# Optimization experiments

Hardware: AMD Instinct MI355X
Metric: run time of the kernel (lower is better)

## Reference

```python
import jax, jax.numpy as jnp
import numpy as np

D_MODEL = 1024
NUM_HEADS = 16
D_HEAD = D_MODEL // NUM_HEADS
MAX_SEQ_LEN = 2048
THETA = 10000.0
BATCH = 2
SEQ = 2048


def _rope_tables():
    # inv_freq over even dims; emb interleaves each freq twice: [f0,f0,f1,f1,...]
    inv_freq = 1.0 / (THETA ** (jnp.arange(0, D_HEAD, 2, dtype=jnp.float32) / D_HEAD))
    t = jnp.arange(MAX_SEQ_LEN, dtype=jnp.float32)
    freqs = jnp.einsum('i,j->ij', t, inv_freq)  # [S, d_head/2]
    emb = jnp.stack((freqs, freqs), axis=-1).reshape(MAX_SEQ_LEN, D_HEAD)
    return jnp.cos(emb), jnp.sin(emb)


def _rotate_half(x):
    # pairwise interleaved rotation: (x0,x1,x2,x3,...) -> (-x1,x0,-x3,x2,...)
    xr = x.reshape(x.shape[:-1] + (D_HEAD // 2, 2))
    x1, x2 = xr[..., 0], xr[..., 1]
    return jnp.stack((-x2, x1), axis=-1).reshape(x.shape)


def setup_inputs() -> dict:
    key = jax.random.key(0)
    ks = jax.random.split(key, 5)
    std = np.sqrt(2.0 / (D_MODEL + D_MODEL)).astype(np.float32)
    return {
        'in_features': jax.random.normal(ks[0], (BATCH, SEQ, D_MODEL), dtype=jnp.float32),
        'token_positions': jnp.arange(SEQ, dtype=jnp.int64) if jax.config.jax_enable_x64 else jnp.arange(SEQ, dtype=jnp.int32),
        'wq': jax.random.normal(ks[1], (D_MODEL, D_MODEL), dtype=jnp.float32) * std,
        'wk': jax.random.normal(ks[2], (D_MODEL, D_MODEL), dtype=jnp.float32) * std,
        'wv': jax.random.normal(ks[3], (D_MODEL, D_MODEL), dtype=jnp.float32) * std,
        'wo': jax.random.normal(ks[4], (D_MODEL, D_MODEL), dtype=jnp.float32) * std,
    }


def reference(in_features, token_positions, wq, wk, wv, wo):
    b, s, _ = in_features.shape
    cos_tab, sin_tab = _rope_tables()
    cos = cos_tab[token_positions]  # [s, d_head]
    sin = sin_tab[token_positions]

    def split_heads(t):  # [b, s, d_model] -> [b, h, s, d_head]
        return t.reshape(b, s, NUM_HEADS, D_HEAD).transpose(0, 2, 1, 3)

    q = split_heads(jnp.einsum('bsd,ed->bse', in_features, wq))
    k = split_heads(jnp.einsum('bsd,ed->bse', in_features, wk))
    v = split_heads(jnp.einsum('bsd,ed->bse', in_features, wv))

    q = q * cos + _rotate_half(q) * sin
    k = k * cos + _rotate_half(k) * sin

    scale = 1.0 / np.sqrt(D_HEAD).astype(np.float32)
    scores = jnp.einsum('bhqd,bhkd->bhqk', q, k) * scale  # [b,h,s,s]
    causal = jnp.tril(jnp.ones((s, s), dtype=bool))
    scores = jnp.where(causal, scores, -jnp.inf)
    weights = jax.nn.softmax(scores, axis=-1)
    out = jnp.einsum('bhqk,bhkd->bhqd', weights, v)
    out = out.transpose(0, 2, 1, 3).reshape(b, s, D_MODEL)
    return jnp.einsum('bsd,ed->bse', out, wo)
```

## Files before the change

### kernel.cpp

```cpp
#include <hip/hip_runtime.h>


typedef __attribute__((ext_vector_type(8))) short bf16x8;
typedef __attribute__((ext_vector_type(4))) float f32x4;

__device__ __forceinline__ short f2bf(float f) {
  unsigned u = __float_as_uint(f);
  unsigned r = (u + 0x7fffu + ((u >> 16) & 1u)) >> 16;
  return (short)(r & 0xFFFFu);
}

__device__ __forceinline__ unsigned pk2(float a, float b) {
  return __builtin_amdgcn_perm(__float_as_uint(b) + 0x8000u,
                               __float_as_uint(a) + 0x8000u, 0x07060302u);
}

__device__ __forceinline__ void async16(const void* g, void* l) {
  __builtin_amdgcn_global_load_lds(
      (const __attribute__((address_space(1))) void*)g,
      (__attribute__((address_space(3))) void*)l, 16, 0, 0);
}

__device__ __forceinline__ void cstore(short* C, size_t i, float v) { C[i] = f2bf(v); }
__device__ __forceinline__ void cstore(float* C, size_t i, float v) { C[i] = v; }

__global__ void cast_all(const float4* __restrict__ X,
                         const float4* __restrict__ w0, const float4* __restrict__ w1,
                         const float4* __restrict__ w2, const float4* __restrict__ w3,
                         short* __restrict__ Xb, short* __restrict__ Wb) {
  int t = blockIdx.x * 256 + threadIdx.x;
  const float4* s;
  short4* d;
  if (t < (1 << 20)) {
    s = X + t; d = (short4*)Xb + t;
  } else {
    int u = t - (1 << 20);
    int which = u >> 18;
    s = ((which == 0) ? w0 : (which == 1) ? w1 : (which == 2) ? w2 : w3) + (u & 0x3FFFF);
    d = (short4*)Wb + u;
  }
  float4 v = *s;
  *d = make_short4(f2bf(v.x), f2bf(v.y), f2bf(v.z), f2bf(v.w));
}

template <typename OUT, int NF, bool ROPE>
__device__ __forceinline__ void gemm_core(const short* __restrict__ A, const short* __restrict__ B,
                                          OUT* __restrict__ C, int bm, int bn, int ldc,
                                          const int* __restrict__ pos) {
  constexpr int BN = 32 * NF;
  __shared__ __align__(16) short As[2][128 * 32];
  __shared__ __align__(16) short Bs[2][BN * 32];
  const int tid  = threadIdx.x;
  const int lane = tid & 63, wave = tid >> 6;
  const int col  = lane & 15, quad = lane >> 4;
  const int wm = (wave & 1) * 64, wn = (wave >> 1) * (16 * NF);

  f32x4 acc[4][NF];
#pragma unroll
  for (int i = 0; i < 4; i++)
#pragma unroll
    for (int j = 0; j < NF; j++) acc[i][j] = (f32x4){0.f, 0.f, 0.f, 0.f};

  auto stage = [&](int k0, int bu) {
#pragma unroll
    for (int c = tid; c < 512; c += 256) {
      int r = c >> 2, cc = (c & 3) << 3;
      async16(A + (size_t)(bm + r) * 1024 + k0 + cc, As[bu] + c * 8);
    }
#pragma unroll
    for (int c = tid; c < BN * 4; c += 256) {
      int r = c >> 2, cc = (c & 3) << 3;
      async16(B + (size_t)(bn + r) * 1024 + k0 + cc, Bs[bu] + c * 8);
    }
  };

  stage(0, 0);
  for (int it = 0; it < 32; ++it) {
    __syncthreads();
    if (it < 31) stage((it + 1) * 32, (it + 1) & 1);
    const short* as = As[it & 1];
    const short* bs = Bs[it & 1];

    bf16x8 af[4], bfr[NF];
#pragma unroll
    for (int i = 0; i < 4; i++)
      af[i] = *(const bf16x8*)(as + (wm + i * 16 + col) * 32 + quad * 8);
#pragma unroll
    for (int i = 0; i < NF; i++)
      bfr[i] = *(const bf16x8*)(bs + (wn + i * 16 + col) * 32 + quad * 8);
#pragma unroll
    for (int mi = 0; mi < 4; mi++)
#pragma unroll
      for (int ni = 0; ni < NF; ni++)
        acc[mi][ni] = __builtin_amdgcn_mfma_f32_16x16x32_bf16(af[mi], bfr[ni], acc[mi][ni], 0, 0, 0);
  }

  if (ROPE) {
    float invf_rev[NF];
#pragma unroll
    for (int ni = 0; ni < NF; ni++) {
      int pr = ((bn + wn + ni * 16 + col) & 63) >> 1;
      invf_rev[ni] = exp2f(-0.4152410118609203f * (float)pr) * 0.15915494309189535f;
    }
    const float sgn = (col & 1) ? 1.f : -1.f;
#pragma unroll
    for (int mi = 0; mi < 4; mi++) {
#pragma unroll
      for (int r = 0; r < 4; r++) {
        int row = bm + wm + mi * 16 + quad * 4 + r;
        float fp = (float)pos[row & 2047];
#pragma unroll
        for (int ni = 0; ni < NF; ni++) {
          float rev = fp * invf_rev[ni];
          rev -= floorf(rev);
          float sn = __builtin_amdgcn_sinf(rev);
          float cs = __builtin_amdgcn_cosf(rev);
          float x  = acc[mi][ni][r];
          float px = __shfl_xor(x, 1);
          acc[mi][ni][r] = fmaf(x, cs, sgn * px * sn);
        }
      }
    }
  }

#pragma unroll
  for (int mi = 0; mi < 4; mi++) {
#pragma unroll
    for (int r = 0; r < 4; r++) {
      size_t row = (size_t)(bm + wm + mi * 16 + quad * 4 + r);
#pragma unroll
      for (int ni = 0; ni < NF; ni++) {
        int cg = bn + wn + ni * 16 + col;
        cstore(C, row * ldc + cg, acc[mi][ni][r]);
      }
    }
  }
}

__global__ __launch_bounds__(256) void qkv_gemm(const short* __restrict__ Xb,
                                                const short* __restrict__ Wq,
                                                const short* __restrict__ Wk,
                                                const short* __restrict__ Wv,
                                                short* __restrict__ Qo,
                                                short* __restrict__ Ko,
                                                short* __restrict__ Vto,
                                                const int* __restrict__ pos) {
  const int z = blockIdx.z;
  if (z == 0)      gemm_core<short, 4, true >(Xb, Wq, Qo, blockIdx.x * 128, blockIdx.y * 128, 1024, pos);
  else if (z == 1) gemm_core<short, 4, true >(Xb, Wk, Ko, blockIdx.x * 128, blockIdx.y * 128, 1024, pos);
  else             gemm_core<short, 4, false>(Wv, Xb, Vto, blockIdx.y * 128, blockIdx.x * 128, 4096, pos);
}

__global__ __launch_bounds__(256) void out_gemm(const short* __restrict__ Ctx,
                                                const short* __restrict__ Wo,
                                                float* __restrict__ C) {
  gemm_core<float, 2, false>(Ctx, Wo, C, blockIdx.x * 128, blockIdx.y * 64, 1024, nullptr);
}

__global__ __launch_bounds__(256) void flash_attn(const short* __restrict__ Q,
                                                  const short* __restrict__ K,
                                                  const short* __restrict__ Vt,
                                                  short* __restrict__ ctx) {
  const int y = blockIdx.y, a = y & 7, kk = y >> 3;
  const int qt = (kk == 0) ? 2 * a : (kk == 1) ? 31 - 2 * a : (kk == 2) ? 2 * a + 1 : 30 - 2 * a;
  const int bh = blockIdx.x;
  const int b = bh >> 4, h = bh & 15;
  __shared__ __align__(16) short Ks[2][64 * 64];
  __shared__ __align__(16) short Vs[2][64 * 64];
  __shared__ __align__(16) short Ps[4][16 * 64];
  const int tid = threadIdx.x, lane = tid & 63, wave = tid >> 6;
  const int col = lane & 15, quad = lane >> 4;

  const size_t qrow = (size_t)(b * 2048 + qt * 64 + wave * 16 + col);
  bf16x8 qf0 = *(const bf16x8*)(Q + qrow * 1024 + h * 64 + quad * 8);
  bf16x8 qf1 = *(const bf16x8*)(Q + qrow * 1024 + h * 64 + 32 + quad * 8);

  float l_i = 0.f;
  f32x4 o_acc[4];
#pragma unroll
  for (int i = 0; i < 4; i++) o_acc[i] = (f32x4){0.f, 0.f, 0.f, 0.f};

  auto stage = [&](int kt, int bu) {
#pragma unroll
    for (int i = 0; i < 2; i++) {
      int c = i * 256 + tid;
      int r = c >> 3;
      int g = ((c & 7) ^ (r & 7)) << 3;
      async16(K  + (size_t)(b * 2048 + kt * 64 + r) * 1024 + h * 64 + g, Ks[bu] + c * 8);
      async16(Vt + (size_t)(h * 64 + r) * 4096 + b * 2048 + kt * 64 + g, Vs[bu] + c * 8);
    }
  };

  int pswr[4], psrd0, psrd1;
#pragma unroll
  for (int nb = 0; nb < 4; nb++) {
    int c8 = nb * 2 + (quad >> 1);
    pswr[nb] = col * 64 + ((c8 ^ (col & 7)) << 3) + (quad & 1) * 4;
  }
  psrd0 = col * 64 + ((quad ^ (col & 7)) << 3);
  psrd1 = col * 64 + (((quad + 4) ^ (col & 7)) << 3);

  const float C1 = 0.18033688011112042f;
  const float C2 = 17.31234049066756f;

  auto tile = [&](int kt, bool diag) {
    const short* ks = Ks[kt & 1];
    const short* vs = Vs[kt & 1];
    f32x4 s_acc[4];
#pragma unroll
    for (int nb = 0; nb < 4; nb++) {
      int row = nb * 16 + col;
      bf16x8 k0 = *(const bf16x8*)(ks + (row * 8 + (quad ^ (row & 7))) * 8);
      bf16x8 k1 = *(const bf16x8*)(ks + (row * 8 + ((quad + 4) ^ (row & 7))) * 8);
      f32x4 z = (f32x4){0.f, 0.f, 0.f, 0.f};
      z = __builtin_amdgcn_mfma_f32_16x16x32_bf16(k0, qf0, z, 0, 0, 0);
      z = __builtin_amdgcn_mfma_f32_16x16x32_bf16(k1, qf1, z, 0, 0, 0);
      s_acc[nb] = z;
    }
#pragma unroll
    for (int nb = 0; nb < 4; nb++) {
      float p[4];
#pragma unroll
      for (int r = 0; r < 4; r++) {
        p[r] = exp2f(s_acc[nb][r] * C1 - C2);
        if (diag && (nb * 16 + quad * 4 + r) > (wave * 16 + col)) p[r] = 0.f;
        l_i += p[r];
      }
      *(uint2*)(&Ps[wave][pswr[nb]]) = make_uint2(pk2(p[0], p[1]), pk2(p[2], p[3]));
    }
    bf16x8 af0 = *(const bf16x8*)(&Ps[wave][psrd0]);
    bf16x8 af1 = *(const bf16x8*)(&Ps[wave][psrd1]);
#pragma unroll
    for (int nb = 0; nb < 4; nb++) {
      int row = nb * 16 + col;
      bf16x8 v0 = *(const bf16x8*)(vs + (row * 8 + (quad ^ (row & 7))) * 8);
      bf16x8 v1 = *(const bf16x8*)(vs + (row * 8 + ((quad + 4) ^ (row & 7))) * 8);
      o_acc[nb] = __builtin_amdgcn_mfma_f32_16x16x32_bf16(af0, v0, o_acc[nb], 0, 0, 0);
      o_acc[nb] = __builtin_amdgcn_mfma_f32_16x16x32_bf16(af1, v1, o_acc[nb], 0, 0, 0);
    }
  };

  stage(0, 0);
  for (int kt = 0; kt < qt; ++kt) {
    __syncthreads();
    stage(kt + 1, (kt + 1) & 1);
    tile(kt, false);
  }
  __syncthreads();
  tile(qt, true);

  l_i += __shfl_xor(l_i, 16);
  l_i += __shfl_xor(l_i, 32);
  float invl = 1.0f / l_i;

#pragma unroll
  for (int r = 0; r < 4; r++) {
    float inv = __shfl(invl, quad * 4 + r);
    size_t row = (size_t)(b * 2048 + qt * 64 + wave * 16 + quad * 4 + r);
#pragma unroll
    for (int nb = 0; nb < 4; nb++)
      ctx[row * 1024 + h * 64 + nb * 16 + col] = f2bf(o_acc[nb][r] * inv);
  }
}

extern "C" void kernel_launch(void* const* d_in, const int* in_sizes, int n_in,
                              void* d_out, int out_size, void* d_ws, size_t ws_size,
                              hipStream_t stream) {
  const float* X  = (const float*)d_in[0];
  const int* pos  = (const int*)d_in[1];
  const float* wq = (const float*)d_in[2];
  const float* wk = (const float*)d_in[3];
  const float* wv = (const float*)d_in[4];
  const float* wo = (const float*)d_in[5];
  float* out = (float*)d_out;

  short* Xb  = (short*)d_ws;
  short* Wqb = Xb + (1 << 22);
  short* Wkb = Wqb + (1 << 20);
  short* Wvb = Wkb + (1 << 20);
  short* Wob = Wvb + (1 << 20);
  short* Qb  = Wob + (1 << 20);
  short* Kb  = Qb + (1 << 22);
  short* Vtb = Kb + (1 << 22);
  short* Ctx = Vtb + (1 << 22);

  cast_all<<<8192, 256, 0, stream>>>((const float4*)X, (const float4*)wq, (const float4*)wk,
                                     (const float4*)wv, (const float4*)wo, Xb, Wqb);
  qkv_gemm<<<dim3(32, 8, 3), 256, 0, stream>>>(Xb, Wqb, Wkb, Wvb, Qb, Kb, Vtb, pos);
  flash_attn<<<dim3(32, 32), 256, 0, stream>>>(Qb, Kb, Vtb, Ctx);
  out_gemm<<<dim3(32, 16), 256, 0, stream>>>(Ctx, Wob, out);
}
```

Baseline: 193.9 us.

## Process 128 query rows per attention block and retile output GEMM to 64x128

The flash attention kernel now gives each wave two 16-row query groups (128 rows per block), so every K/V tile staged in shared memory is reused across twice as many queries and the grid is halved. Causal masking spans two diagonal key tiles, and the P scratch buffer uses a padded 72-element row stride instead of an XOR swizzle. The output GEMM switches from 128x64 to 64x128 tiles, with shared memory moved to kernel scope. The cost is more registers per wave and fewer blocks to balance the triangular causal work, which could reduce occupancy.

```diff
diff --git a/kernel.cpp b/kernel.cpp
--- a/kernel.cpp
+++ b/kernel.cpp
@@ -43,34 +43,33 @@
   *d = make_short4(f2bf(v.x), f2bf(v.y), f2bf(v.z), f2bf(v.w));
 }
 
-template <typename OUT, int NF, bool ROPE>
-__device__ __forceinline__ void gemm_core(const short* __restrict__ A, const short* __restrict__ B,
+template <typename OUT, int MR, int NR, bool ROPE>
+__device__ __forceinline__ void gemm_core(short* __restrict__ As, short* __restrict__ Bs,
+                                          const short* __restrict__ A, const short* __restrict__ B,
                                           OUT* __restrict__ C, int bm, int bn, int ldc,
                                           const int* __restrict__ pos) {
-  constexpr int BN = 32 * NF;
-  __shared__ __align__(16) short As[2][128 * 32];
-  __shared__ __align__(16) short Bs[2][BN * 32];
+  constexpr int BM = 32 * MR, BN = 32 * NR;
   const int tid  = threadIdx.x;
   const int lane = tid & 63, wave = tid >> 6;
   const int col  = lane & 15, quad = lane >> 4;
-  const int wm = (wave & 1) * 64, wn = (wave >> 1) * (16 * NF);
-
-  f32x4 acc[4][NF];
-#pragma unroll
-  for (int i = 0; i < 4; i++)
-#pragma unroll
-    for (int j = 0; j < NF; j++) acc[i][j] = (f32x4){0.f, 0.f, 0.f, 0.f};
+  const int wm = (wave & 1) * (16 * MR), wn = (wave >> 1) * (16 * NR);
+
+  f32x4 acc[MR][NR];
+#pragma unroll
+  for (int i = 0; i < MR; i++)
+#pragma unroll
+    for (int j = 0; j < NR; j++) acc[i][j] = (f32x4){0.f, 0.f, 0.f, 0.f};
 
   auto stage = [&](int k0, int bu) {
 #pragma unroll
-    for (int c = tid; c < 512; c += 256) {
+    for (int c = tid; c < BM * 4; c += 256) {
       int r = c >> 2, cc = (c & 3) << 3;
-      async16(A + (size_t)(bm + r) * 1024 + k0 + cc, As[bu] + c * 8);
+      async16(A + (size_t)(bm + r) * 1024 + k0 + cc, As + bu * BM * 32 + c * 8);
     }
 #pragma unroll
     for (int c = tid; c < BN * 4; c += 256) {
       int r = c >> 2, cc = (c & 3) << 3;
-      async16(B + (size_t)(bn + r) * 1024 + k0 + cc, Bs[bu] + c * 8);
+      async16(B + (size_t)(bn + r) * 1024 + k0 + cc, Bs + bu * BN * 32 + c * 8);
     }
   };
 
@@ -78,39 +77,39 @@
   for (int it = 0; it < 32; ++it) {
     __syncthreads();
     if (it < 31) stage((it + 1) * 32, (it + 1) & 1);
-    const short* as = As[it & 1];
-    const short* bs = Bs[it & 1];
-
-    bf16x8 af[4], bfr[NF];
-#pragma unroll
-    for (int i = 0; i < 4; i++)
+    const short* as = As + (it & 1) * BM * 32;
+    const short* bs = Bs + (it & 1) * BN * 32;
+
+    bf16x8 af[MR], bfr[NR];
+#pragma unroll
+    for (int i = 0; i < MR; i++)
       af[i] = *(const bf16x8*)(as + (wm + i * 16 + col) * 32 + quad * 8);
 #pragma unroll
-    for (int i = 0; i < NF; i++)
+    for (int i = 0; i < NR; i++)
       bfr[i] = *(const bf16x8*)(bs + (wn + i * 16 + col) * 32 + quad * 8);
 #pragma unroll
-    for (int mi = 0; mi < 4; mi++)
-#pragma unroll
-      for (int ni = 0; ni < NF; ni++)
+    for (int mi = 0; mi < MR; mi++)
+#pragma unroll
+      for (int ni = 0; ni < NR; ni++)
         acc[mi][ni] = __builtin_amdgcn_mfma_f32_16x16x32_bf16(af[mi], bfr[ni], acc[mi][ni], 0, 0, 0);
   }
 
   if (ROPE) {
-    float invf_rev[NF];
-#pragma unroll
-    for (int ni = 0; ni < NF; ni++) {
+    float invf_rev[NR];
+#pragma unroll
+    for (int ni = 0; ni < NR; ni++) {
       int pr = ((bn + wn + ni * 16 + col) & 63) >> 1;
       invf_rev[ni] = exp2f(-0.4152410118609203f * (float)pr) * 0.15915494309189535f;
     }
     const float sgn = (col & 1) ? 1.f : -1.f;
 #pragma unroll
-    for (int mi = 0; mi < 4; mi++) {
+    for (int mi = 0; mi < MR; mi++) {
 #pragma unroll
       for (int r = 0; r < 4; r++) {
         int row = bm + wm + mi * 16 + quad * 4 + r;
         float fp = (float)pos[row & 2047];
 #pragma unroll
-        for (int ni = 0; ni < NF; ni++) {
+        for (int ni = 0; ni < NR; ni++) {
           float rev = fp * invf_rev[ni];
           rev -= floorf(rev);
           float sn = __builtin_amdgcn_sinf(rev);
@@ -124,12 +123,12 @@
   }
 
 #pragma unroll
-  for (int mi = 0; mi < 4; mi++) {
+  for (int mi = 0; mi < MR; mi++) {
 #pragma unroll
     for (int r = 0; r < 4; r++) {
       size_t row = (size_t)(bm + wm + mi * 16 + quad * 4 + r);
 #pragma unroll
-      for (int ni = 0; ni < NF; ni++) {
+      for (int ni = 0; ni < NR; ni++) {
         int cg = bn + wn + ni * 16 + col;
         cstore(C, row * ldc + cg, acc[mi][ni][r]);
       }
@@ -145,40 +144,51 @@
                                                 short* __restrict__ Ko,
                                                 short* __restrict__ Vto,
                                                 const int* __restrict__ pos) {
+  __shared__ __align__(16) short sm[2 * 128 * 32 + 2 * 128 * 32];
+  short* As = sm;
+  short* Bs = sm + 2 * 128 * 32;
   const int z = blockIdx.z;
-  if (z == 0)      gemm_core<short, 4, true >(Xb, Wq, Qo, blockIdx.x * 128, blockIdx.y * 128, 1024, pos);
-  else if (z == 1) gemm_core<short, 4, true >(Xb, Wk, Ko, blockIdx.x * 128, blockIdx.y * 128, 1024, pos);
-  else             gemm_core<short, 4, false>(Wv, Xb, Vto, blockIdx.y * 128, blockIdx.x * 128, 4096, pos);
+  if (z == 0)      gemm_core<short, 4, 4, true >(As, Bs, Xb, Wq, Qo, blockIdx.x * 128, blockIdx.y * 128, 1024, pos);
+  else if (z == 1) gemm_core<short, 4, 4, true >(As, Bs, Xb, Wk, Ko, blockIdx.x * 128, blockIdx.y * 128, 1024, pos);
+  else             gemm_core<short, 4, 4, false>(As, Bs, Wv, Xb, Vto, blockIdx.y * 128, blockIdx.x * 128, 4096, pos);
 }
 
 __global__ __launch_bounds__(256) void out_gemm(const short* __restrict__ Ctx,
                                                 const short* __restrict__ Wo,
                                                 float* __restrict__ C) {
-  gemm_core<float, 2, false>(Ctx, Wo, C, blockIdx.x * 128, blockIdx.y * 64, 1024, nullptr);
+  __shared__ __align__(16) short sm[2 * 64 * 32 + 2 * 128 * 32];
+  gemm_core<float, 2, 4, false>(sm, sm + 2 * 64 * 32, Ctx, Wo, C,
+                                blockIdx.x * 64, blockIdx.y * 128, 1024, nullptr);
 }
 
 __global__ __launch_bounds__(256) void flash_attn(const short* __restrict__ Q,
                                                   const short* __restrict__ K,
                                                   const short* __restrict__ Vt,
                                                   short* __restrict__ ctx) {
-  const int y = blockIdx.y, a = y & 7, kk = y >> 3;
-  const int qt = (kk == 0) ? 2 * a : (kk == 1) ? 31 - 2 * a : (kk == 2) ? 2 * a + 1 : 30 - 2 * a;
+  const int y = blockIdx.y;
+  const int qt = (y < 8) ? y : 23 - y;
   const int bh = blockIdx.x;
   const int b = bh >> 4, h = bh & 15;
   __shared__ __align__(16) short Ks[2][64 * 64];
   __shared__ __align__(16) short Vs[2][64 * 64];
-  __shared__ __align__(16) short Ps[4][16 * 64];
+  __shared__ __align__(16) short Ps[4][32 * 72];
   const int tid = threadIdx.x, lane = tid & 63, wave = tid >> 6;
   const int col = lane & 15, quad = lane >> 4;
 
-  const size_t qrow = (size_t)(b * 2048 + qt * 64 + wave * 16 + col);
-  bf16x8 qf0 = *(const bf16x8*)(Q + qrow * 1024 + h * 64 + quad * 8);
-  bf16x8 qf1 = *(const bf16x8*)(Q + qrow * 1024 + h * 64 + 32 + quad * 8);
-
-  float l_i = 0.f;
-  f32x4 o_acc[4];
-#pragma unroll
-  for (int i = 0; i < 4; i++) o_acc[i] = (f32x4){0.f, 0.f, 0.f, 0.f};
+  bf16x8 qf[2][2];
+#pragma unroll
+  for (int g = 0; g < 2; g++) {
+    const size_t qrow = (size_t)(b * 2048 + qt * 128 + wave * 32 + g * 16 + col);
+    qf[g][0] = *(const bf16x8*)(Q + qrow * 1024 + h * 64 + quad * 8);
+    qf[g][1] = *(const bf16x8*)(Q + qrow * 1024 + h * 64 + 32 + quad * 8);
+  }
+
+  float l_i[2] = {0.f, 0.f};
+  f32x4 o_acc[2][4];
+#pragma unroll
+  for (int g = 0; g < 2; g++)
+#pragma unroll
+    for (int i = 0; i < 4; i++) o_acc[g][i] = (f32x4){0.f, 0.f, 0.f, 0.f};
 
   auto stage = [&](int kt, int bu) {
 #pragma unroll
@@ -191,75 +201,90 @@
     }
   };
 
-  int pswr[4], psrd0, psrd1;
-#pragma unroll
-  for (int nb = 0; nb < 4; nb++) {
-    int c8 = nb * 2 + (quad >> 1);
-    pswr[nb] = col * 64 + ((c8 ^ (col & 7)) << 3) + (quad & 1) * 4;
-  }
-  psrd0 = col * 64 + ((quad ^ (col & 7)) << 3);
-  psrd1 = col * 64 + (((quad + 4) ^ (col & 7)) << 3);
-
   const float C1 = 0.18033688011112042f;
   const float C2 = 17.31234049066756f;
 
   auto tile = [&](int kt, bool diag) {
     const short* ks = Ks[kt & 1];
     const short* vs = Vs[kt & 1];
-    f32x4 s_acc[4];
+    f32x4 s_acc[2][4];
 #pragma unroll
     for (int nb = 0; nb < 4; nb++) {
       int row = nb * 16 + col;
       bf16x8 k0 = *(const bf16x8*)(ks + (row * 8 + (quad ^ (row & 7))) * 8);
       bf16x8 k1 = *(const bf16x8*)(ks + (row * 8 + ((quad + 4) ^ (row & 7))) * 8);
-      f32x4 z = (f32x4){0.f, 0.f, 0.f, 0.f};
-      z = __builtin_amdgcn_mfma_f32_16x16x32_bf16(k0, qf0, z, 0, 0, 0);
-      z = __builtin_amdgcn_mfma_f32_16x16x32_bf16(k1, qf1, z, 0, 0, 0);
-      s_acc[nb] = z;
-    }
-#pragma unroll
-    for (int nb = 0; nb < 4; nb++) {
-      float p[4];
-#pragma unroll
-      for (int r = 0; r < 4; r++) {
-        p[r] = exp2f(s_acc[nb][r] * C1 - C2);
-        if (diag && (nb * 16 + quad * 4 + r) > (wave * 16 + col)) p[r] = 0.f;
-        l_i += p[r];
-      }
-      *(uint2*)(&Ps[wave][pswr[nb]]) = make_uint2(pk2(p[0], p[1]), pk2(p[2], p[3]));
-    }
-    bf16x8 af0 = *(const bf16x8*)(&Ps[wave][psrd0]);
-    bf16x8 af1 = *(const bf16x8*)(&Ps[wave][psrd1]);
+#pragma unroll
+      for (int g = 0; g < 2; g++) {
+        f32x4 z = (f32x4){0.f, 0.f, 0.f, 0.f};
+        z = __builtin_amdgcn_mfma_f32_16x16x32_bf16(k0, qf[g][0], z, 0, 0, 0);
+        z = __builtin_amdgcn_mfma_f32_16x16x32_bf16(k1, qf[g][1], z, 0, 0, 0);
+        s_acc[g][nb] = z;
+      }
+    }
+#pragma unroll
+    for (int g = 0; g < 2; g++) {
+#pragma unroll
+      for (int nb = 0; nb < 4; nb++) {
+        float p[4];
+#pragma unroll
+        for (int r = 0; r < 4; r++) {
+          p[r] = exp2f(s_acc[g][nb][r] * C1 - C2);
+          if (diag) {
+            int key = kt * 64 + nb * 16 + quad * 4 + r;
+            int qg  = qt * 128 + wave * 32 + g * 16 + col;
+            if (key > qg) p[r] = 0.f;
+          }
+          l_i[g] += p[r];
+        }
+        *(uint2*)(&Ps[wave][(g * 16 + col) * 72 + nb * 16 + quad * 4]) =
+            make_uint2(pk2(p[0], p[1]), pk2(p[2], p[3]));
+      }
+    }
+    bf16x8 af[2][2];
+#pragma unroll
+    for (int g = 0; g < 2; g++) {
+      af[g][0] = *(const bf16x8*)(&Ps[wave][(g * 16 + col) * 72 + quad * 8]);
+      af[g][1] = *(const bf16x8*)(&Ps[wave][(g * 16 + col) * 72 + 32 + quad * 8]);
+    }
 #pragma unroll
     for (int nb = 0; nb < 4; nb++) {
       int row = nb * 16 + col;
       bf16x8 v0 = *(const bf16x8*)(vs + (row * 8 + (quad ^ (row & 7))) * 8);
       bf16x8 v1 = *(const bf16x8*)(vs + (row * 8 + ((quad + 4) ^ (row & 7))) * 8);
-      o_acc[nb] = __builtin_amdgcn_mfma_f32_16x16x32_bf16(af0, v0, o_acc[nb], 0, 0, 0);
-      o_acc[nb] = __builtin_amdgcn_mfma_f32_16x16x32_bf16(af1, v1, o_acc[nb], 0, 0, 0);
+#pragma unroll
+      for (int g = 0; g < 2; g++) {
+        o_acc[g][nb] = __builtin_amdgcn_mfma_f32_16x16x32_bf16(af[g][0], v0, o_acc[g][nb], 0, 0, 0);
+        o_acc[g][nb] = __builtin_amdgcn_mfma_f32_16x16x32_bf16(af[g][1], v1, o_acc[g][nb], 0, 0, 0);
+      }
     }
   };
 
+  const int last = 2 * qt + 1;
   stage(0, 0);
-  for (int kt = 0; kt < qt; ++kt) {
+  for (int kt = 0; kt <= last; ++kt) {
     __syncthreads();
-    stage(kt + 1, (kt + 1) & 1);
-    tile(kt, false);
-  }
-  __syncthreads();
-  tile(qt, true);
-
-  l_i += __shfl_xor(l_i, 16);
-  l_i += __shfl_xor(l_i, 32);
-  float invl = 1.0f / l_i;
-
-#pragma unroll
-  for (int r = 0; r < 4; r++) {
-    float inv = __shfl(invl, quad * 4 + r);
-    size_t row = (size_t)(b * 2048 + qt * 64 + wave * 16 + quad * 4 + r);
-#pragma unroll
-    for (int nb = 0; nb < 4; nb++)
-      ctx[row * 1024 + h * 64 + nb * 16 + col] = f2bf(o_acc[nb][r] * inv);
+    if (kt < last) stage(kt + 1, (kt + 1) & 1);
+    if (kt < 2 * qt)                   tile(kt, false);
+    else if (wave >= 2 || kt == 2 * qt) tile(kt, true);
+  }
+
+#pragma unroll
+  for (int g = 0; g < 2; g++) {
+    l_i[g] += __shfl_xor(l_i[g], 16);
+    l_i[g] += __shfl_xor(l_i[g], 32);
+  }
+
+#pragma unroll
+  for (int g = 0; g < 2; g++) {
+    float invl = 1.0f / l_i[g];
+#pragma unroll
+    for (int r = 0; r < 4; r++) {
+      float inv = __shfl(invl, quad * 4 + r);
+      size_t row = (size_t)(b * 2048 + qt * 128 + wave * 32 + g * 16 + quad * 4 + r);
+#pragma unroll
+      for (int nb = 0; nb < 4; nb++)
+        ctx[row * 1024 + h * 64 + nb * 16 + col] = f2bf(o_acc[g][nb][r] * inv);
+    }
   }
 }
 
@@ -287,6 +312,6 @@
   cast_all<<<8192, 256, 0, stream>>>((const float4*)X, (const float4*)wq, (const float4*)wk,
                                      (const float4*)wv, (const float4*)wo, Xb, Wqb);
   qkv_gemm<<<dim3(32, 8, 3), 256, 0, stream>>>(Xb, Wqb, Wkb, Wvb, Qb, Kb, Vtb, pos);
-  flash_attn<<<dim3(32, 32), 256, 0, stream>>>(Qb, Kb, Vtb, Ctx);
-  out_gemm<<<dim3(32, 16), 256, 0, stream>>>(Ctx, Wob, out);
-}
+  flash_attn<<<dim3(32, 16), 256, 0, stream>>>(Qb, Kb, Vtb, Ctx);
+  out_gemm<<<dim3(64, 8), 256, 0, stream>>>(Ctx, Wob, out);
+}
```

New measurement: 194.1 us. About the same (+0.1%).
